# Performance work log

Hardware: AMD Instinct MI355X
Metric: run time of the kernel (lower is better)

Reference implementation:

```python
import jax, jax.numpy as jnp
import numpy as np

B_ = 2; L_ = 4096; D_MODEL = 1024; D_INNER = 2048; D_STATE = 128
N_HEADS = 32; HEADDIM = 64; D_CONV = 4; CHUNK = 64
CONV_DIM = D_INNER + 2 * D_STATE
EPS = 1e-5


def silu(x):
    return x * jax.nn.sigmoid(x)


def segsum(x):
    # x: (..., T) -> (..., T, T) stable segment sums; exp() gives 1-semiseparable matrix
    T = x.shape[-1]
    xe = jnp.broadcast_to(x[..., None], x.shape + (T,))  # (..., T, T)
    lower = jnp.tril(jnp.ones((T, T), bool), -1)
    xs = jnp.cumsum(jnp.where(lower, xe, 0.0), axis=-2)
    incl = jnp.tril(jnp.ones((T, T), bool), 0)
    return jnp.where(incl, xs, -jnp.inf)


def ssd(x, A, Bm, Cm):
    # x: (b, l, h, p); A: (b, l, h); Bm/Cm: (b, l, n) (single shared head, as in module)
    b, l, h, p = x.shape
    c = l // CHUNK
    x = x.reshape(b, c, CHUNK, h, p)
    A = A.reshape(b, c, CHUNK, h).transpose(0, 3, 1, 2)  # (b, h, c, l)
    Bm = Bm.reshape(b, c, CHUNK, D_STATE)
    Cm = Cm.reshape(b, c, CHUNK, D_STATE)
    A_cumsum = jnp.cumsum(A, axis=-1)                    # (b, h, c, l)
    Lmat = jnp.exp(segsum(A))                            # (b, h, c, l, l)
    # intra-chunk (diagonal blocks)
    Y_diag = jnp.einsum('bcln,bcsn,bhcls,bcshp->bclhp', Cm, Bm, Lmat, x)
    # per-chunk states
    decay_states = jnp.exp(A_cumsum[:, :, :, -1:] - A_cumsum)  # (b, h, c, l)
    states = jnp.einsum('bcln,bhcl,bclhp->bchpn', Bm, decay_states, x)
    init = jnp.zeros_like(states[:, :1])
    states = jnp.concatenate([init, states], axis=1)     # (b, c+1, h, p, n)
    A_last = jnp.pad(A_cumsum[:, :, :, -1], ((0, 0), (0, 0), (1, 0)))  # (b, h, c+1)
    decay_chunk = jnp.exp(segsum(A_last))                # (b, h, c+1, c+1)
    new_states = jnp.einsum('bhzc,bchpn->bzhpn', decay_chunk, states)
    states_prev = new_states[:, :-1]                     # (b, c, h, p, n)
    state_decay_out = jnp.exp(A_cumsum)
    Y_off = jnp.einsum('bcln,bchpn,bhcl->bclhp', Cm, states_prev, state_decay_out)
    return (Y_diag + Y_off).reshape(b, l, h, p)


def setup_inputs() -> dict:
    key = jax.random.key(0)
    ks = jax.random.split(key, 9)
    u = jax.random.normal(ks[0], (B_, L_, D_MODEL), jnp.float32)
    W_in = jax.random.normal(ks[1], (2 * D_INNER + 2 * D_STATE + N_HEADS, D_MODEL), jnp.float32) * (D_MODEL ** -0.5)
    conv_w = jax.random.normal(ks[2], (CONV_DIM, 1, D_CONV), jnp.float32) * 0.2
    conv_b = jax.random.normal(ks[3], (CONV_DIM,), jnp.float32) * 0.02
    dt_bias = jax.random.normal(ks[4], (N_HEADS,), jnp.float32) * 0.1
    A_log = jnp.log(jax.random.uniform(ks[5], (N_HEADS,), jnp.float32, 1.0, 16.0))
    D_param = jax.random.normal(ks[6], (N_HEADS,), jnp.float32) * 0.5
    norm_w = jnp.ones((D_INNER,), jnp.float32)
    W_out = jax.random.normal(ks[7], (D_MODEL, D_INNER), jnp.float32) * (D_INNER ** -0.5)
    return dict(u=u, W_in=W_in, conv_w=conv_w, conv_b=conv_b, dt_bias=dt_bias,
                A_log=A_log, D_param=D_param, norm_w=norm_w, W_out=W_out)


def mamba_forward(u, W_in, conv_w, conv_b, dt_bias, A_log, D_param, norm_w, W_out):
    b, l, _ = u.shape
    zxbcdt = u @ W_in.T                                  # (b, l, 2*di+2*ds+h)
    z = zxbcdt[..., :D_INNER]
    xBC = zxbcdt[..., D_INNER:D_INNER + CONV_DIM]
    dt = zxbcdt[..., D_INNER + CONV_DIM:]
    dt = jax.nn.softplus(dt + dt_bias)                   # (b, l, h)
    # causal depthwise conv1d
    xc = jnp.transpose(xBC, (0, 2, 1))                   # (b, conv_dim, l)
    xc = jax.lax.conv_general_dilated(xc, conv_w, (1,), [(D_CONV - 1, 0)],
                                      feature_group_count=CONV_DIM,
                                      dimension_numbers=('NCH', 'OIH', 'NCH'))
    xc = xc + conv_b[None, :, None]
    xBC = silu(jnp.transpose(xc, (0, 2, 1)))             # (b, l, conv_dim)
    x = xBC[..., :D_INNER]
    Bc = xBC[..., D_INNER:D_INNER + D_STATE]
    Cc = xBC[..., D_INNER + D_STATE:]
    x = x.reshape(b, l, N_HEADS, HEADDIM)
    A = -jnp.exp(A_log)                                  # (h,)
    Y = ssd(x * dt[..., None], A * dt, Bc, Cc)           # (b, l, h, p)
    y = Y + x * D_param[:, None]
    y = y.reshape(b, l, D_INNER)
    # gated RMSNorm
    y = y * silu(z)
    y = y * jax.lax.rsqrt(jnp.mean(y * y, axis=-1, keepdims=True) + EPS) * norm_w
    return y @ W_out.T


def reference(u, W_in, conv_w, conv_b, dt_bias, A_log, D_param, norm_w, W_out):
    return mamba_forward(u, W_in, conv_w, conv_b, dt_bias, A_log, D_param, norm_w, W_out)
```

## Files before the change

kernel.cpp:

```cpp
#include <hip/hip_runtime.h>
#include <hip/hip_bf16.h>
#include <math.h>

#define B_    2
#define L_    4096
#define DM    1024
#define DI    2048
#define DS    128
#define NH    32
#define HD    64
#define CHUNK 64
#define NC    (L_/CHUNK)
#define CD    (DI + 2*DS)
#define ROWS  (B_*L_)
#define NOUT  (2*DI + 2*DS + NH)
#define NPAD2 4608

typedef __attribute__((ext_vector_type(4))) float f32x4;
typedef __attribute__((ext_vector_type(8))) __bf16 bf16x8;
typedef __attribute__((ext_vector_type(4))) short s16x4;
typedef __attribute__((ext_vector_type(8))) short s16x8;

__global__ __launch_bounds__(256) void k_convert_all(const float* __restrict__ u, const float* __restrict__ W_in,
                                                     const float* __restrict__ W_out, __bf16* __restrict__ ubf,
                                                     __bf16* __restrict__ wibf, __bf16* __restrict__ wobf) {
    int i = blockIdx.x * 256 + threadIdx.x;
    const int QU  = ROWS * DM / 4;
    const int QWI = NPAD2 * DM / 4;
    const int QWO = DM * DI / 4;
    const float* s = nullptr;
    __bf16* d;
    bool zero = false;
    if (i < QU) {
        s = u + (size_t)i * 4; d = ubf + (size_t)i * 4;
    } else if (i < QU + QWI) {
        int j = i - QU;
        d = wibf + (size_t)j * 4;
        if (j < NOUT * DM / 4) s = W_in + (size_t)j * 4; else zero = true;
    } else if (i < QU + QWI + QWO) {
        int j = i - QU - QWI;
        s = W_out + (size_t)j * 4; d = wobf + (size_t)j * 4;
    } else return;
    s16x4 o = {0, 0, 0, 0};
    if (!zero) {
        f32x4 v = *(const f32x4*)s;
#pragma unroll
        for (int q = 0; q < 4; q++) o[q] = __builtin_bit_cast(short, (__bf16)v[q]);
    }
    *(s16x4*)d = o;
}

__device__ __forceinline__ void stage_half(const __bf16* __restrict__ G, int ldg, int grow0, int kt,
                                           char* lds, int ldsoff, int tid, int wave) {
#pragma unroll
    for (int issue = 0; issue < 2; issue++) {
        int o   = issue * 8192 + tid * 16;
        int row = o >> 7;
        int cb  = (o & 127) ^ ((row & 7) << 4);
        const __bf16* src = G + (size_t)(grow0 + row) * ldg + kt + (cb >> 1);
        char* ldsbase = lds + ldsoff + issue * 8192 + wave * 1024;
        __builtin_amdgcn_global_load_lds((const __attribute__((address_space(1))) void*)src,
                                         (__attribute__((address_space(3))) void*)ldsbase,
                                         16, 0, 0);
    }
}

__device__ __forceinline__ bf16x8 rdfrag(const char* lds, int ldsoff, int r, int ks, int lane) {
    int logical = r * 128 + ks * 64 + ((lane >> 4) << 4);
    int phys    = logical ^ ((r & 7) << 4);
    return *(const bf16x8*)(lds + ldsoff + phys);
}

#define MFMA_CLUSTER(AF, BF, ACC)                                                         \
    __builtin_amdgcn_s_setprio(1);                                                       \
    _Pragma("unroll")                                                                    \
    for (int fm = 0; fm < 4; fm++)                                                       \
        _Pragma("unroll")                                                                \
        for (int fn = 0; fn < 2; fn++)                                                   \
            _Pragma("unroll")                                                            \
            for (int ks = 0; ks < 2; ks++)                                               \
                ACC[fm][fn] = __builtin_amdgcn_mfma_f32_16x16x32_bf16(AF[fm][ks], BF[fn][ks], ACC[fm][fn], 0, 0, 0); \
    __builtin_amdgcn_s_setprio(0);

__device__ __forceinline__ void gemm128x256_core(const __bf16* __restrict__ Ag, const __bf16* __restrict__ Bg,
                                                 int K, int m0, int n0, char* lds, f32x4 acc[4][4]) {
    const int tid = threadIdx.x, wave = tid >> 6, lane = tid & 63;
    const int wm = wave >> 2, wn = wave & 3, lrow = lane & 15;
    const int KT = K >> 6;
    const int brow = wn * 64;
    const int bhalf = 16384 + ((brow >> 7) << 14);
    const int brl = brow & 127;

    for (int t = 0; t < KT; t++) {
        const int kt = t << 6;
        stage_half(Ag, K, m0,       kt, lds, 0,     tid, wave);
        stage_half(Bg, K, n0,       kt, lds, 16384, tid, wave);
        stage_half(Bg, K, n0 + 128, kt, lds, 32768, tid, wave);
        asm volatile("s_waitcnt vmcnt(0)" ::: "memory");
        __builtin_amdgcn_s_barrier();
        bf16x8 a[4][2];
#pragma unroll
        for (int fm = 0; fm < 4; fm++)
#pragma unroll
            for (int ks = 0; ks < 2; ks++)
                a[fm][ks] = rdfrag(lds, 0, wm * 64 + fm * 16 + lrow, ks, lane);
        __builtin_amdgcn_s_setprio(1);
#pragma unroll
        for (int fn = 0; fn < 4; fn++) {
            bf16x8 b0 = rdfrag(lds, bhalf, brl + fn * 16 + lrow, 0, lane);
            bf16x8 b1 = rdfrag(lds, bhalf, brl + fn * 16 + lrow, 1, lane);
#pragma unroll
            for (int fm = 0; fm < 4; fm++) {
                acc[fm][fn] = __builtin_amdgcn_mfma_f32_16x16x32_bf16(a[fm][0], b0, acc[fm][fn], 0, 0, 0);
                acc[fm][fn] = __builtin_amdgcn_mfma_f32_16x16x32_bf16(a[fm][1], b1, acc[fm][fn], 0, 0, 0);
            }
        }
        __builtin_amdgcn_s_setprio(0);
        __builtin_amdgcn_s_barrier();
    }
}

__device__ __forceinline__ void gemm256x128_core(const __bf16* __restrict__ Ag, const __bf16* __restrict__ Bg,
                                                 int K, int m0, int n0, char* lds, f32x4 acc[8][2]) {
    const int tid = threadIdx.x, wave = tid >> 6, lane = tid & 63;
    const int wmq = wave >> 2, wnq = wave & 3, lrow = lane & 15;
    const int KT = K >> 6;
    const int aoff = wmq * 16384;

    auto stage_tile = [&](int t, int p) {
        const int kt = t << 6;
        stage_half(Ag, K, m0,       kt, lds, p * 49152,         tid, wave);
        stage_half(Ag, K, m0 + 128, kt, lds, p * 49152 + 16384, tid, wave);
        stage_half(Bg, K, n0,       kt, lds, p * 49152 + 32768, tid, wave);
    };
    stage_tile(0, 0);
    asm volatile("s_waitcnt vmcnt(0)" ::: "memory");
    __builtin_amdgcn_s_barrier();

    bf16x8 ra[4][2], rb[2][2];
#pragma unroll
    for (int fm = 0; fm < 4; fm++)
#pragma unroll
        for (int ks = 0; ks < 2; ks++)
            ra[fm][ks] = rdfrag(lds, aoff, fm * 16 + lrow, ks, lane);
#pragma unroll
    for (int fn = 0; fn < 2; fn++)
#pragma unroll
        for (int ks = 0; ks < 2; ks++)
            rb[fn][ks] = rdfrag(lds, 32768, wnq * 32 + fn * 16 + lrow, ks, lane);

    for (int t = 0; t < KT; t++) {
        const int p = t & 1, pn = p ^ 1;
        const bool dsg = (t + 1 < KT);
        if (dsg) {
            stage_half(Ag, K, m0,       (t + 1) << 6, lds, pn * 49152,         tid, wave);
            stage_half(Ag, K, m0 + 128, (t + 1) << 6, lds, pn * 49152 + 16384, tid, wave);
        }
        {
            f32x4 (*a0)[2] = &acc[0];
            MFMA_CLUSTER(ra, rb, a0);
        }
#pragma unroll
        for (int fm = 0; fm < 4; fm++)
#pragma unroll
            for (int ks = 0; ks < 2; ks++)
                ra[fm][ks] = rdfrag(lds, p * 49152 + aoff, 64 + fm * 16 + lrow, ks, lane);
        if (dsg) stage_half(Bg, K, n0, (t + 1) << 6, lds, pn * 49152 + 32768, tid, wave);
        {
            f32x4 (*a1)[2] = &acc[4];
            MFMA_CLUSTER(ra, rb, a1);
        }
        asm volatile("s_waitcnt vmcnt(0)" ::: "memory");
        __builtin_amdgcn_s_barrier();
        if (dsg) {
#pragma unroll
            for (int fm = 0; fm < 4; fm++)
#pragma unroll
                for (int ks = 0; ks < 2; ks++)
                    ra[fm][ks] = rdfrag(lds, pn * 49152 + aoff, fm * 16 + lrow, ks, lane);
#pragma unroll
            for (int fn = 0; fn < 2; fn++)
#pragma unroll
                for (int ks = 0; ks < 2; ks++)
                    rb[fn][ks] = rdfrag(lds, pn * 49152 + 32768, wnq * 32 + fn * 16 + lrow, ks, lane);
        }
    }
}

__global__ __launch_bounds__(512, 4) void k_gemm1(const __bf16* __restrict__ ubf, const __bf16* __restrict__ wibf,
                                                  __bf16* __restrict__ zbuf, __bf16* __restrict__ xbcraw,
                                                  float* __restrict__ dtbuf, const float* __restrict__ dt_bias) {
    extern __shared__ char lds[];
    f32x4 acc[4][4];
    f32x4 z4 = {0.f, 0.f, 0.f, 0.f};
#pragma unroll
    for (int i = 0; i < 4; i++)
#pragma unroll
        for (int j = 0; j < 4; j++) acc[i][j] = z4;

    int bid = blockIdx.x;
    int wg  = (bid & 7) * 144 + (bid >> 3);
    int m0  = (wg / 18) * 128;
    int n0  = (wg % 18) * 256;
    gemm128x256_core(ubf, wibf, DM, m0, n0, lds, acc);

    const int lane = threadIdx.x & 63, wave = threadIdx.x >> 6;
    const int wm = wave >> 2, wn = wave & 3;
    const int gm_base = m0 + wm * 64 + ((lane >> 4) << 2);
    const int gn_base = n0 + wn * 64 + (lane & 15);
#pragma unroll
    for (int fm = 0; fm < 4; fm++) {
        const int gmb = gm_base + fm * 16;
#pragma unroll
        for (int fn = 0; fn < 4; fn++) {
            const int gn = gn_base + fn * 16;
            if (gn < DI) {
#pragma unroll
                for (int r = 0; r < 4; r++)
                    zbuf[(size_t)(gmb + r) * DI + gn] = (__bf16)acc[fm][fn][r];
            } else if (gn < DI + CD) {
#pragma unroll
                for (int r = 0; r < 4; r++)
                    xbcraw[(size_t)(gmb + r) * CD + (gn - DI)] = (__bf16)acc[fm][fn][r];
            } else if (gn < NOUT) {
                const int hh = gn - (DI + CD);
                const float bb = dt_bias[hh];
#pragma unroll
                for (int r = 0; r < 4; r++) {
                    float x = acc[fm][fn][r] + bb;
                    float sp = (x > 20.f) ? x : log1pf(__expf(x));
                    dtbuf[(size_t)(gmb + r) * NH + hh] = sp;
                }
            }
        }
    }
}

__global__ __launch_bounds__(512, 2) void k_gemm2(const __bf16* __restrict__ ybf, const __bf16* __restrict__ wobf,
                                                  float* __restrict__ out) {
    extern __shared__ char lds[];
    f32x4 acc[8][2];
    f32x4 z4 = {0.f, 0.f, 0.f, 0.f};
#pragma unroll
    for (int i = 0; i < 8; i++)
#pragma unroll
        for (int j = 0; j < 2; j++) acc[i][j] = z4;

    int bid = blockIdx.x;
    int wg  = (bid & 7) * 32 + (bid >> 3);
    int m0  = (wg / 8) * 256;
    int n0  = (wg % 8) * 128;
    gemm256x128_core(ybf, wobf, DI, m0, n0, lds, acc);

    const int lane = threadIdx.x & 63, wave = threadIdx.x >> 6;
    const int wmq = wave >> 2, wnq = wave & 3;
#pragma unroll
    for (int fm = 0; fm < 8; fm++) {
        const int gmb = m0 + wmq * 128 + fm * 16 + ((lane >> 4) << 2);
#pragma unroll
        for (int fn = 0; fn < 2; fn++) {
            const int gn = n0 + wnq * 32 + fn * 16 + (lane & 15);
#pragma unroll
            for (int r = 0; r < 4; r++)
                out[(size_t)(gmb + r) * DM + gn] = acc[fm][fn][r];
        }
    }
}

__global__ __launch_bounds__(256) void k_conv(const __bf16* __restrict__ xbcraw, const float* __restrict__ conv_w,
                                              const float* __restrict__ conv_b, __bf16* __restrict__ xconv) {
    __shared__ float wsh[256 * 4];
    __shared__ float bsh[256];
    const int tid  = threadIdx.x;
    const int gsub = tid & 31;
    const int roct = tid >> 5;
    const int ch_base_blk = blockIdx.x * 256;
    *(f32x4*)&wsh[tid * 4] = *(const f32x4*)&conv_w[ch_base_blk * 4 + tid * 4];
    bsh[tid] = conv_b[ch_base_blk + tid];
    __syncthreads();

    const int ch0  = ch_base_blk + gsub * 8;
    const int row0 = (blockIdx.y * 8 + roct) * 8;
    const int l0   = row0 & (L_ - 1);
    const __bf16* src = xbcraw + (size_t)row0 * CD + ch0;

    s16x8 rr[11];
#pragma unroll
    for (int j = 0; j < 11; j++) {
        int ll = l0 - 3 + j;
        if (ll >= 0) rr[j] = *(const s16x8*)(src + (size_t)(j - 3) * CD);
        else         rr[j] = (s16x8){0, 0, 0, 0, 0, 0, 0, 0};
    }

    const int chl = gsub * 8;
    float w[8][4], bias[8];
#pragma unroll
    for (int j = 0; j < 8; j++) {
        bias[j] = bsh[chl + j];
#pragma unroll
        for (int k = 0; k < 4; k++) w[j][k] = wsh[(chl + j) * 4 + k];
    }

    __bf16* dst = xconv + (size_t)row0 * CD + ch0;
#pragma unroll
    for (int orow = 0; orow < 8; orow++) {
        float a[8];
#pragma unroll
        for (int j = 0; j < 8; j++) a[j] = bias[j];
#pragma unroll
        for (int k = 0; k < 4; k++) {
            s16x8 v = rr[orow + k];
#pragma unroll
            for (int j = 0; j < 8; j++)
                a[j] += w[j][k] * (float)__builtin_bit_cast(__bf16, (short)v[j]);
        }
        s16x8 o;
#pragma unroll
        for (int j = 0; j < 8; j++)
            o[j] = __builtin_bit_cast(short, (__bf16)(a[j] * __builtin_amdgcn_rcpf(1.f + __expf(-a[j]))));
        *(s16x8*)(dst + (size_t)orow * CD) = o;
    }
}

__global__ __launch_bounds__(256) void k_cbt(const __bf16* __restrict__ xconv, float* __restrict__ cbt) {
    const int c = blockIdx.x, b = blockIdx.y;
    const int tid = threadIdx.x, wv = tid >> 6, lane = tid & 63;
    const int lrow = lane & 15, lko = (lane >> 4) * 8;
    __shared__ __align__(16) __bf16 Csh[64 * 136];
    __shared__ __align__(16) __bf16 Bsh[64 * 136];
    const size_t rowbase = (size_t)b * L_ + c * CHUNK;
#pragma unroll
    for (int q = 0; q < 32; q++) {
        int i = q * 2 + (wv >> 1);
        int n = (wv & 1) * 64 + lane;
        const __bf16* base = xconv + (rowbase + i) * CD + DI;
        Bsh[i * 136 + n] = base[n];
        Csh[i * 136 + n] = base[DS + n];
    }
    __syncthreads();
    f32x4 acc[4];
    f32x4 z4 = {0.f, 0.f, 0.f, 0.f};
#pragma unroll
    for (int jt = 0; jt < 4; jt++) acc[jt] = z4;
#pragma unroll
    for (int ks = 0; ks < 4; ks++) {
        bf16x8 a = *(const bf16x8*)&Csh[(wv * 16 + lrow) * 136 + ks * 32 + lko];
#pragma unroll
        for (int jt = 0; jt < 4; jt++) {
            bf16x8 bb = *(const bf16x8*)&Bsh[(jt * 16 + lrow) * 136 + ks * 32 + lko];
            acc[jt] = __builtin_amdgcn_mfma_f32_16x16x32_bf16(a, bb, acc[jt], 0, 0, 0);
        }
    }
    float* o = cbt + (size_t)(b * NC + c) * 4096;
#pragma unroll
    for (int jt = 0; jt < 4; jt++)
#pragma unroll
        for (int r = 0; r < 4; r++) {
            int i = wv * 16 + (lane >> 4) * 4 + r;
            int j = jt * 16 + lrow;
            o[i * 64 + j] = acc[jt][r];
        }
}

__global__ __launch_bounds__(256) void k_ssd_a(const __bf16* __restrict__ xconv, const float* __restrict__ dtbuf,
                                               const float* __restrict__ cbt, const float* __restrict__ A_log,
                                               __bf16* __restrict__ ybuf, __bf16* __restrict__ states,
                                               float* __restrict__ asum, const float* __restrict__ D_param) {
    const int hg = blockIdx.x, c = blockIdx.y, b = blockIdx.z;
    const int tid = threadIdx.x, wv = tid >> 6, lane = tid & 63;
    const int lrow = lane & 15, lko = (lane >> 4) * 8;
    __shared__ __align__(16) __bf16 xT[64 * 72];
    __shared__ __align__(16) __bf16 xsc[64 * 72];
    __shared__ __align__(16) __bf16 BT[128 * 72];
    __shared__ __align__(16) __bf16 Ms[64 * 72];
    __shared__ float dts[64], cum[64];

    const size_t rowbase = (size_t)b * L_ + c * CHUNK;
#pragma unroll
    for (int q = 0; q < 32; q++) {
        int i = q * 2 + (wv >> 1);
        int n = (wv & 1) * 64 + lane;
        BT[n * 72 + i] = xconv[(rowbase + i) * CD + DI + n];
    }
    const float* cbt_bc = cbt + (size_t)(b * NC + c) * 4096;
    f32x4 z4 = {0.f, 0.f, 0.f, 0.f};

    for (int hh = 0; hh < 8; hh++) {
        const int h = hg * 8 + hh;
        const float Ah = -__expf(A_log[h]);
        const float Dh = D_param[h];
#pragma unroll
        for (int q = 0; q < 16; q++) {
            int i = q * 4 + wv;
            xT[lane * 72 + i] = xconv[(rowbase + i) * CD + h * HD + lane];
        }
        if (wv == 0) {
            float dtv = dtbuf[(rowbase + lane) * NH + h];
            dts[lane] = dtv;
            float v = Ah * dtv;
#pragma unroll
            for (int o = 1; o < 64; o <<= 1) { float t = __shfl_up(v, o); if (lane >= o) v += t; }
            cum[lane] = v;
            if (lane == 63) asum[(b * NC + c) * NH + h] = v;
        }
        __syncthreads();

        const float cum63 = cum[63];
#pragma unroll
        for (int q = 0; q < 16; q++) {
            int i = q * 4 + wv, j = lane;
            float cumi = cum[i];
            float m = 0.f;
            if (j <= i) m = cbt_bc[i * 64 + j] * __expf(cumi - cum[j]) * dts[j];
            if (j == i) m += Dh;
            Ms[i * 72 + j] = (__bf16)m;
            float dcfi = __expf(cum63 - cumi) * dts[i];
            xsc[lane * 72 + i] = (__bf16)((float)xT[lane * 72 + i] * dcfi);
        }
        __syncthreads();

        {
            f32x4 accY[4];
#pragma unroll
            for (int pt = 0; pt < 4; pt++) accY[pt] = z4;
#pragma unroll
            for (int ks = 0; ks < 2; ks++) {
                bf16x8 a = *(const bf16x8*)&Ms[(wv * 16 + lrow) * 72 + ks * 32 + lko];
#pragma unroll
                for (int pt = 0; pt < 4; pt++) {
                    bf16x8 bb = *(const bf16x8*)&xT[(pt * 16 + lrow) * 72 + ks * 32 + lko];
                    accY[pt] = __builtin_amdgcn_mfma_f32_16x16x32_bf16(a, bb, accY[pt], 0, 0, 0);
                }
            }
#pragma unroll
            for (int pt = 0; pt < 4; pt++)
#pragma unroll
                for (int r = 0; r < 4; r++) {
                    int i = wv * 16 + (lane >> 4) * 4 + r;
                    int p = pt * 16 + lrow;
                    ybuf[(rowbase + i) * DI + h * HD + p] = (__bf16)accY[pt][r];
                }
        }
        {
            f32x4 accS[8];
#pragma unroll
            for (int nt = 0; nt < 8; nt++) accS[nt] = z4;
#pragma unroll
            for (int ks = 0; ks < 2; ks++) {
                bf16x8 a = *(const bf16x8*)&xsc[(wv * 16 + lrow) * 72 + ks * 32 + lko];
#pragma unroll
                for (int nt = 0; nt < 8; nt++) {
                    bf16x8 bb = *(const bf16x8*)&BT[(nt * 16 + lrow) * 72 + ks * 32 + lko];
                    accS[nt] = __builtin_amdgcn_mfma_f32_16x16x32_bf16(a, bb, accS[nt], 0, 0, 0);
                }
            }
            __bf16* sp = states + ((size_t)(b * NC + c) * NH + h) * 8192;
#pragma unroll
            for (int nt = 0; nt < 8; nt++)
#pragma unroll
                for (int r = 0; r < 4; r++) {
                    int p = wv * 16 + (lane >> 4) * 4 + r;
                    int n = nt * 16 + lrow;
                    sp[p * 128 + n] = (__bf16)accS[nt][r];
                }
        }
        __syncthreads();
    }
}

__global__ __launch_bounds__(256) void k_scan(__bf16* __restrict__ states, const float* __restrict__ asum) {
    const int seg = blockIdx.x, h = blockIdx.y, b = blockIdx.z;
    __shared__ float efs[NC];
    if (threadIdx.x < NC) efs[threadIdx.x] = __expf(asum[(b * NC + threadIdx.x) * NH + h]);
    __syncthreads();
    const int e0 = seg * 1024 + threadIdx.x * 4;
    __bf16* base = states + ((size_t)(b * NC) * NH + h) * 8192 + e0;
    const size_t cs = (size_t)NH * 8192;
    float S[4] = {0.f, 0.f, 0.f, 0.f};
    s16x4 r0 = *(const s16x4*)(base);
    s16x4 r1 = *(const s16x4*)(base + cs);
    s16x4 r2 = *(const s16x4*)(base + 2 * cs);
    s16x4 r3;
#define SCAN_STEP(RV, CC)                                                                  \
    {                                                                                      \
        s16x4 o; float e = efs[CC];                                                        \
        _Pragma("unroll")                                                                  \
        for (int q = 0; q < 4; q++) {                                                      \
            float t = (float)__builtin_bit_cast(__bf16, (short)RV[q]);                     \
            o[q] = __builtin_bit_cast(short, (__bf16)S[q]);                                \
            S[q] = e * S[q] + t;                                                           \
        }                                                                                  \
        *(s16x4*)(base + (size_t)(CC) * cs) = o;                                           \
    }
    for (int c = 0; c < NC; c += 4) {
        r3 = *(const s16x4*)(base + (size_t)(c + 3) * cs);
        SCAN_STEP(r0, c);
        if (c + 4 < NC) r0 = *(const s16x4*)(base + (size_t)(c + 4) * cs);
        SCAN_STEP(r1, c + 1);
        if (c + 5 < NC) r1 = *(const s16x4*)(base + (size_t)(c + 5) * cs);
        SCAN_STEP(r2, c + 2);
        if (c + 6 < NC) r2 = *(const s16x4*)(base + (size_t)(c + 6) * cs);
        SCAN_STEP(r3, c + 3);
    }
#undef SCAN_STEP
}

__global__ __launch_bounds__(256) void k_ssd_b(const __bf16* __restrict__ xconv, const float* __restrict__ dtbuf,
                                               const __bf16* __restrict__ states, const float* __restrict__ A_log,
                                               __bf16* __restrict__ ybuf) {
    const int hg = blockIdx.x, c = blockIdx.y, b = blockIdx.z;
    const int tid = threadIdx.x, wv = tid >> 6, lane = tid & 63;
    const int lrow = lane & 15, lko = (lane >> 4) * 8;
    __shared__ __align__(16) __bf16 Csh[64 * 136];
    __shared__ __align__(16) __bf16 Sps[64 * 136];
    __shared__ float cum[64];

    const size_t rowbase = (size_t)b * L_ + c * CHUNK;
#pragma unroll
    for (int q = 0; q < 32; q++) {
        int i = q * 2 + (wv >> 1);
        int n = (wv & 1) * 64 + lane;
        Csh[i * 136 + n] = xconv[(rowbase + i) * CD + DI + DS + n];
    }
    f32x4 z4 = {0.f, 0.f, 0.f, 0.f};

    for (int hh = 0; hh < 8; hh++) {
        const int h = hg * 8 + hh;
        const float Ah = -__expf(A_log[h]);
        const __bf16* sp = states + ((size_t)(b * NC + c) * NH + h) * 8192;
#pragma unroll
        for (int q = 0; q < 32; q++) {
            int i = q * 2 + (wv >> 1);
            int n = (wv & 1) * 64 + lane;
            Sps[i * 136 + n] = sp[i * 128 + n];
        }
        if (wv == 0) {
            float v = Ah * dtbuf[(rowbase + lane) * NH + h];
#pragma unroll
            for (int o = 1; o < 64; o <<= 1) { float t = __shfl_up(v, o); if (lane >= o) v += t; }
            cum[lane] = v;
        }
        __syncthreads();

        f32x4 acc[4];
#pragma unroll
        for (int pt = 0; pt < 4; pt++) acc[pt] = z4;
#pragma unroll
        for (int ks = 0; ks < 4; ks++) {
            bf16x8 a = *(const bf16x8*)&Csh[(wv * 16 + lrow) * 136 + ks * 32 + lko];
#pragma unroll
            for (int pt = 0; pt < 4; pt++) {
                bf16x8 bb = *(const bf16x8*)&Sps[(pt * 16 + lrow) * 136 + ks * 32 + lko];
                acc[pt] = __builtin_amdgcn_mfma_f32_16x16x32_bf16(a, bb, acc[pt], 0, 0, 0);
            }
        }
#pragma unroll
        for (int r = 0; r < 4; r++) {
            int i = wv * 16 + (lane >> 4) * 4 + r;
            float ef = __expf(cum[i]);
#pragma unroll
            for (int pt = 0; pt < 4; pt++) {
                size_t idx = (rowbase + i) * DI + h * HD + pt * 16 + lrow;
                float y0 = (float)ybuf[idx];
                ybuf[idx] = (__bf16)(y0 + ef * acc[pt][r]);
            }
        }
        __syncthreads();
    }
}

__global__ __launch_bounds__(256) void k_gate_norm(const __bf16* __restrict__ ybuf, const __bf16* __restrict__ zbuf,
                                                   const float* __restrict__ norm_w, __bf16* __restrict__ ybf) {
    const int r = blockIdx.x;
    const int tid = threadIdx.x;
    const int col0 = tid * 8;
    s16x8 y8 = *(const s16x8*)(ybuf + (size_t)r * DI + col0);
    s16x8 z8 = *(const s16x8*)(zbuf + (size_t)r * DI + col0);
    float v[8];
    float ss = 0.f;
#pragma unroll
    for (int q = 0; q < 8; q++) {
        float y = (float)__builtin_bit_cast(__bf16, (short)y8[q]);
        float z = (float)__builtin_bit_cast(__bf16, (short)z8[q]);
        float g = z * __builtin_amdgcn_rcpf(1.f + __expf(-z));
        v[q] = y * g;
        ss += v[q] * v[q];
    }
#pragma unroll
    for (int o = 32; o > 0; o >>= 1) ss += __shfl_down(ss, o);
    __shared__ float wsum[4];
    __shared__ float rmss;
    if ((tid & 63) == 0) wsum[tid >> 6] = ss;
    __syncthreads();
    if (tid == 0) {
        float t = wsum[0] + wsum[1] + wsum[2] + wsum[3];
        rmss = rsqrtf(t / (float)DI + 1e-5f);
    }
    __syncthreads();
    float rm = rmss;
    s16x8 o8;
#pragma unroll
    for (int q = 0; q < 8; q++)
        o8[q] = __builtin_bit_cast(short, (__bf16)(v[q] * rm * norm_w[col0 + q]));
    *(s16x8*)(ybf + (size_t)r * DI + col0) = o8;
}

extern "C" void kernel_launch(void* const* d_in, const int* in_sizes, int n_in,
                              void* d_out, int out_size, void* d_ws, size_t ws_size,
                              hipStream_t stream) {
    const float* u       = (const float*)d_in[0];
    const float* W_in    = (const float*)d_in[1];
    const float* conv_w  = (const float*)d_in[2];
    const float* conv_b  = (const float*)d_in[3];
    const float* dt_bias = (const float*)d_in[4];
    const float* A_log   = (const float*)d_in[5];
    const float* D_param = (const float*)d_in[6];
    const float* norm_w  = (const float*)d_in[7];
    const float* W_out   = (const float*)d_in[8];
    float* out = (float*)d_out;

    constexpr size_t OFF_WOBF  = 0;
    constexpr size_t OFF_ZBUF  = 4194304;
    constexpr size_t OFF_DT    = 37748736;
    constexpr size_t OFF_ASUM  = 38797312;
    constexpr size_t OFF_XCONV = 38813696;
    constexpr size_t OFF_CBT   = 76562432;
    constexpr size_t OFF_BIG   = 78659584;
    constexpr size_t NEED      = 145768448;
    if (ws_size < NEED) return;

    char* ws = (char*)d_ws;
    __bf16* wobf   = (__bf16*)(ws + OFF_WOBF);
    __bf16* zbuf   = (__bf16*)(ws + OFF_ZBUF);
    float*  dtbuf  = (float*) (ws + OFF_DT);
    float*  asum   = (float*) (ws + OFF_ASUM);
    __bf16* xconv  = (__bf16*)(ws + OFF_XCONV);
    float*  cbt    = (float*) (ws + OFF_CBT);
    __bf16* ubf    = (__bf16*)(ws + OFF_BIG);
    __bf16* wibf   = (__bf16*)(ws + OFF_BIG + 16777216);
    __bf16* xbcraw = (__bf16*)(ws + OFF_BIG + 16777216 + 9437184);
    __bf16* states = (__bf16*)(ws + OFF_BIG);
    __bf16* ybf    = (__bf16*)(ws + OFF_XCONV);
    __bf16* ybuf   = (__bf16*)d_out;

    (void)hipFuncSetAttribute((const void*)k_gemm1, hipFuncAttributeMaxDynamicSharedMemorySize, 49152);
    (void)hipFuncSetAttribute((const void*)k_gemm2, hipFuncAttributeMaxDynamicSharedMemorySize, 98304);

    constexpr int QTOT = ROWS * DM / 4 + NPAD2 * DM / 4 + DM * DI / 4;
    k_convert_all<<<(QTOT + 255) / 256, 256, 0, stream>>>(u, W_in, W_out, ubf, wibf, wobf);

    k_gemm1<<<1152, 512, 49152, stream>>>(ubf, wibf, zbuf, xbcraw, dtbuf, dt_bias);
    k_conv<<<dim3(9, 128), 256, 0, stream>>>(xbcraw, conv_w, conv_b, xconv);
    k_cbt<<<dim3(NC, B_), 256, 0, stream>>>(xconv, cbt);
    k_ssd_a<<<dim3(4, NC, B_), 256, 0, stream>>>(xconv, dtbuf, cbt, A_log, ybuf, states, asum, D_param);
    k_scan<<<dim3(8, NH, B_), 256, 0, stream>>>(states, asum);
    k_ssd_b<<<dim3(4, NC, B_), 256, 0, stream>>>(xconv, dtbuf, states, A_log, ybuf);
    k_gate_norm<<<ROWS, 256, 0, stream>>>(ybuf, zbuf, norm_w, ybf);
    k_gemm2<<<256, 512, 98304, stream>>>(ybf, wobf, out);
}
```

Baseline: 369.4 us.

## Launch one block per head in SSD kernels and shrink gemm2 tiles

The SSD intra-chunk and state-output kernels now run one block per (head, chunk, batch) instead of looping over 8 heads per block. This gives 8x more blocks and removes the per-head barriers, at the cost of reloading the shared B and C chunk data once per head. The output GEMM swaps the double-buffered 256x128 tile for a simpler single-buffered 128x128 tile with less LDS and higher occupancy, so twice as many blocks launch but the load/compute overlap is lost.

```diff
diff --git a/kernel.cpp b/kernel.cpp
--- a/kernel.cpp
+++ b/kernel.cpp
@@ -71,17 +71,6 @@
     return *(const bf16x8*)(lds + ldsoff + phys);
 }
 
-#define MFMA_CLUSTER(AF, BF, ACC)                                                         \
-    __builtin_amdgcn_s_setprio(1);                                                       \
-    _Pragma("unroll")                                                                    \
-    for (int fm = 0; fm < 4; fm++)                                                       \
-        _Pragma("unroll")                                                                \
-        for (int fn = 0; fn < 2; fn++)                                                   \
-            _Pragma("unroll")                                                            \
-            for (int ks = 0; ks < 2; ks++)                                               \
-                ACC[fm][fn] = __builtin_amdgcn_mfma_f32_16x16x32_bf16(AF[fm][ks], BF[fn][ks], ACC[fm][fn], 0, 0, 0); \
-    __builtin_amdgcn_s_setprio(0);
-
 __device__ __forceinline__ void gemm128x256_core(const __bf16* __restrict__ Ag, const __bf16* __restrict__ Bg,
                                                  int K, int m0, int n0, char* lds, f32x4 acc[4][4]) {
     const int tid = threadIdx.x, wave = tid >> 6, lane = tid & 63;
@@ -120,70 +109,37 @@
     }
 }
 
-__device__ __forceinline__ void gemm256x128_core(const __bf16* __restrict__ Ag, const __bf16* __restrict__ Bg,
-                                                 int K, int m0, int n0, char* lds, f32x4 acc[8][2]) {
+__device__ __forceinline__ void gemm128x128_core(const __bf16* __restrict__ Ag, const __bf16* __restrict__ Bg,
+                                                 int K, int m0, int n0, char* lds, f32x4 acc[4][2]) {
     const int tid = threadIdx.x, wave = tid >> 6, lane = tid & 63;
-    const int wmq = wave >> 2, wnq = wave & 3, lrow = lane & 15;
+    const int wm = wave >> 2, wn = wave & 3, lrow = lane & 15;
     const int KT = K >> 6;
-    const int aoff = wmq * 16384;
-
-    auto stage_tile = [&](int t, int p) {
+
+    for (int t = 0; t < KT; t++) {
         const int kt = t << 6;
-        stage_half(Ag, K, m0,       kt, lds, p * 49152,         tid, wave);
-        stage_half(Ag, K, m0 + 128, kt, lds, p * 49152 + 16384, tid, wave);
-        stage_half(Bg, K, n0,       kt, lds, p * 49152 + 32768, tid, wave);
-    };
-    stage_tile(0, 0);
-    asm volatile("s_waitcnt vmcnt(0)" ::: "memory");
-    __builtin_amdgcn_s_barrier();
-
-    bf16x8 ra[4][2], rb[2][2];
-#pragma unroll
-    for (int fm = 0; fm < 4; fm++)
-#pragma unroll
-        for (int ks = 0; ks < 2; ks++)
-            ra[fm][ks] = rdfrag(lds, aoff, fm * 16 + lrow, ks, lane);
-#pragma unroll
-    for (int fn = 0; fn < 2; fn++)
-#pragma unroll
-        for (int ks = 0; ks < 2; ks++)
-            rb[fn][ks] = rdfrag(lds, 32768, wnq * 32 + fn * 16 + lrow, ks, lane);
-
-    for (int t = 0; t < KT; t++) {
-        const int p = t & 1, pn = p ^ 1;
-        const bool dsg = (t + 1 < KT);
-        if (dsg) {
-            stage_half(Ag, K, m0,       (t + 1) << 6, lds, pn * 49152,         tid, wave);
-            stage_half(Ag, K, m0 + 128, (t + 1) << 6, lds, pn * 49152 + 16384, tid, wave);
-        }
-        {
-            f32x4 (*a0)[2] = &acc[0];
-            MFMA_CLUSTER(ra, rb, a0);
-        }
-#pragma unroll
-        for (int fm = 0; fm < 4; fm++)
-#pragma unroll
-            for (int ks = 0; ks < 2; ks++)
-                ra[fm][ks] = rdfrag(lds, p * 49152 + aoff, 64 + fm * 16 + lrow, ks, lane);
-        if (dsg) stage_half(Bg, K, n0, (t + 1) << 6, lds, pn * 49152 + 32768, tid, wave);
-        {
-            f32x4 (*a1)[2] = &acc[4];
-            MFMA_CLUSTER(ra, rb, a1);
-        }
+        stage_half(Ag, K, m0, kt, lds, 0,     tid, wave);
+        stage_half(Bg, K, n0, kt, lds, 16384, tid, wave);
         asm volatile("s_waitcnt vmcnt(0)" ::: "memory");
         __builtin_amdgcn_s_barrier();
-        if (dsg) {
-#pragma unroll
-            for (int fm = 0; fm < 4; fm++)
-#pragma unroll
-                for (int ks = 0; ks < 2; ks++)
-                    ra[fm][ks] = rdfrag(lds, pn * 49152 + aoff, fm * 16 + lrow, ks, lane);
-#pragma unroll
-            for (int fn = 0; fn < 2; fn++)
-#pragma unroll
-                for (int ks = 0; ks < 2; ks++)
-                    rb[fn][ks] = rdfrag(lds, pn * 49152 + 32768, wnq * 32 + fn * 16 + lrow, ks, lane);
-        }
+        bf16x8 a[4][2];
+#pragma unroll
+        for (int fm = 0; fm < 4; fm++)
+#pragma unroll
+            for (int ks = 0; ks < 2; ks++)
+                a[fm][ks] = rdfrag(lds, 0, wm * 64 + fm * 16 + lrow, ks, lane);
+        __builtin_amdgcn_s_setprio(1);
+#pragma unroll
+        for (int fn = 0; fn < 2; fn++) {
+            bf16x8 b0 = rdfrag(lds, 16384, wn * 32 + fn * 16 + lrow, 0, lane);
+            bf16x8 b1 = rdfrag(lds, 16384, wn * 32 + fn * 16 + lrow, 1, lane);
+#pragma unroll
+            for (int fm = 0; fm < 4; fm++) {
+                acc[fm][fn] = __builtin_amdgcn_mfma_f32_16x16x32_bf16(a[fm][0], b0, acc[fm][fn], 0, 0, 0);
+                acc[fm][fn] = __builtin_amdgcn_mfma_f32_16x16x32_bf16(a[fm][1], b1, acc[fm][fn], 0, 0, 0);
+            }
+        }
+        __builtin_amdgcn_s_setprio(0);
+        __builtin_amdgcn_s_barrier();
     }
 }
 
@@ -236,30 +192,32 @@
     }
 }
 
-__global__ __launch_bounds__(512, 2) void k_gemm2(const __bf16* __restrict__ ybf, const __bf16* __restrict__ wobf,
+__global__ __launch_bounds__(512, 4) void k_gemm2(const __bf16* __restrict__ ybf, const __bf16* __restrict__ wobf,
                                                   float* __restrict__ out) {
     extern __shared__ char lds[];
-    f32x4 acc[8][2];
+    f32x4 acc[4][2];
     f32x4 z4 = {0.f, 0.f, 0.f, 0.f};
 #pragma unroll
-    for (int i = 0; i < 8; i++)
+    for (int i = 0; i < 4; i++)
 #pragma unroll
         for (int j = 0; j < 2; j++) acc[i][j] = z4;
 
     int bid = blockIdx.x;
-    int wg  = (bid & 7) * 32 + (bid >> 3);
-    int m0  = (wg / 8) * 256;
+    int wg  = (bid & 7) * 64 + (bid >> 3);
+    int m0  = (wg / 8) * 128;
     int n0  = (wg % 8) * 128;
-    gemm256x128_core(ybf, wobf, DI, m0, n0, lds, acc);
+    gemm128x128_core(ybf, wobf, DI, m0, n0, lds, acc);
 
     const int lane = threadIdx.x & 63, wave = threadIdx.x >> 6;
-    const int wmq = wave >> 2, wnq = wave & 3;
-#pragma unroll
-    for (int fm = 0; fm < 8; fm++) {
-        const int gmb = m0 + wmq * 128 + fm * 16 + ((lane >> 4) << 2);
+    const int wm = wave >> 2, wn = wave & 3;
+    const int gm_base = m0 + wm * 64 + ((lane >> 4) << 2);
+    const int gn_base = n0 + wn * 32 + (lane & 15);
+#pragma unroll
+    for (int fm = 0; fm < 4; fm++) {
+        const int gmb = gm_base + fm * 16;
 #pragma unroll
         for (int fn = 0; fn < 2; fn++) {
-            const int gn = n0 + wnq * 32 + fn * 16 + (lane & 15);
+            const int gn = gn_base + fn * 16;
 #pragma unroll
             for (int r = 0; r < 4; r++)
                 out[(size_t)(gmb + r) * DM + gn] = acc[fm][fn][r];
@@ -366,7 +324,7 @@
                                                const float* __restrict__ cbt, const float* __restrict__ A_log,
                                                __bf16* __restrict__ ybuf, __bf16* __restrict__ states,
                                                float* __restrict__ asum, const float* __restrict__ D_param) {
-    const int hg = blockIdx.x, c = blockIdx.y, b = blockIdx.z;
+    const int h = blockIdx.x, c = blockIdx.y, b = blockIdx.z;
     const int tid = threadIdx.x, wv = tid >> 6, lane = tid & 63;
     const int lrow = lane & 15, lko = (lane >> 4) * 8;
     __shared__ __align__(16) __bf16 xT[64 * 72];
@@ -375,96 +333,92 @@
     __shared__ __align__(16) __bf16 Ms[64 * 72];
     __shared__ float dts[64], cum[64];
 
+    const float Ah = -__expf(A_log[h]);
     const size_t rowbase = (size_t)b * L_ + c * CHUNK;
+
+    float dtv = 0.f;
+    if (wv == 0) { dtv = dtbuf[(rowbase + lane) * NH + h]; dts[lane] = dtv; }
+#pragma unroll
+    for (int q = 0; q < 16; q++) {
+        int i = q * 4 + wv;
+        xT[lane * 72 + i] = xconv[(rowbase + i) * CD + h * HD + lane];
+    }
 #pragma unroll
     for (int q = 0; q < 32; q++) {
         int i = q * 2 + (wv >> 1);
         int n = (wv & 1) * 64 + lane;
         BT[n * 72 + i] = xconv[(rowbase + i) * CD + DI + n];
     }
+    if (wv == 0) {
+        float v = Ah * dtv;
+#pragma unroll
+        for (int o = 1; o < 64; o <<= 1) { float t = __shfl_up(v, o); if (lane >= o) v += t; }
+        cum[lane] = v;
+        if (lane == 63) asum[(b * NC + c) * NH + h] = v;
+    }
+    __syncthreads();
+
+    const float cum63 = cum[63];
+    const float Dh = D_param[h];
     const float* cbt_bc = cbt + (size_t)(b * NC + c) * 4096;
+#pragma unroll
+    for (int q = 0; q < 16; q++) {
+        int i = q * 4 + wv, j = lane;
+        float cumi = cum[i];
+        float m = 0.f;
+        if (j <= i) m = cbt_bc[i * 64 + j] * __expf(cumi - cum[j]) * dts[j];
+        if (j == i) m += Dh;
+        Ms[i * 72 + j] = (__bf16)m;
+        float dcfi = __expf(cum63 - cumi) * dts[i];
+        xsc[lane * 72 + i] = (__bf16)((float)xT[lane * 72 + i] * dcfi);
+    }
+    __syncthreads();
+
     f32x4 z4 = {0.f, 0.f, 0.f, 0.f};
-
-    for (int hh = 0; hh < 8; hh++) {
-        const int h = hg * 8 + hh;
-        const float Ah = -__expf(A_log[h]);
-        const float Dh = D_param[h];
-#pragma unroll
-        for (int q = 0; q < 16; q++) {
-            int i = q * 4 + wv;
-            xT[lane * 72 + i] = xconv[(rowbase + i) * CD + h * HD + lane];
-        }
-        if (wv == 0) {
-            float dtv = dtbuf[(rowbase + lane) * NH + h];
-            dts[lane] = dtv;
-            float v = Ah * dtv;
-#pragma unroll
-            for (int o = 1; o < 64; o <<= 1) { float t = __shfl_up(v, o); if (lane >= o) v += t; }
-            cum[lane] = v;
-            if (lane == 63) asum[(b * NC + c) * NH + h] = v;
-        }
-        __syncthreads();
-
-        const float cum63 = cum[63];
-#pragma unroll
-        for (int q = 0; q < 16; q++) {
-            int i = q * 4 + wv, j = lane;
-            float cumi = cum[i];
-            float m = 0.f;
-            if (j <= i) m = cbt_bc[i * 64 + j] * __expf(cumi - cum[j]) * dts[j];
-            if (j == i) m += Dh;
-            Ms[i * 72 + j] = (__bf16)m;
-            float dcfi = __expf(cum63 - cumi) * dts[i];
-            xsc[lane * 72 + i] = (__bf16)((float)xT[lane * 72 + i] * dcfi);
-        }
-        __syncthreads();
-
-        {
-            f32x4 accY[4];
-#pragma unroll
-            for (int pt = 0; pt < 4; pt++) accY[pt] = z4;
-#pragma unroll
-            for (int ks = 0; ks < 2; ks++) {
-                bf16x8 a = *(const bf16x8*)&Ms[(wv * 16 + lrow) * 72 + ks * 32 + lko];
-#pragma unroll
-                for (int pt = 0; pt < 4; pt++) {
-                    bf16x8 bb = *(const bf16x8*)&xT[(pt * 16 + lrow) * 72 + ks * 32 + lko];
-                    accY[pt] = __builtin_amdgcn_mfma_f32_16x16x32_bf16(a, bb, accY[pt], 0, 0, 0);
-                }
+    {
+        f32x4 accY[4];
+#pragma unroll
+        for (int pt = 0; pt < 4; pt++) accY[pt] = z4;
+#pragma unroll
+        for (int ks = 0; ks < 2; ks++) {
+            bf16x8 a = *(const bf16x8*)&Ms[(wv * 16 + lrow) * 72 + ks * 32 + lko];
+#pragma unroll
+            for (int pt = 0; pt < 4; pt++) {
+                bf16x8 bb = *(const bf16x8*)&xT[(pt * 16 + lrow) * 72 + ks * 32 + lko];
+                accY[pt] = __builtin_amdgcn_mfma_f32_16x16x32_bf16(a, bb, accY[pt], 0, 0, 0);
             }
-#pragma unroll
-            for (int pt = 0; pt < 4; pt++)
-#pragma unroll
-                for (int r = 0; r < 4; r++) {
-                    int i = wv * 16 + (lane >> 4) * 4 + r;
-                    int p = pt * 16 + lrow;
-                    ybuf[(rowbase + i) * DI + h * HD + p] = (__bf16)accY[pt][r];
-                }
-        }
-        {
-            f32x4 accS[8];
-#pragma unroll
-            for (int nt = 0; nt < 8; nt++) accS[nt] = z4;
-#pragma unroll
-            for (int ks = 0; ks < 2; ks++) {
-                bf16x8 a = *(const bf16x8*)&xsc[(wv * 16 + lrow) * 72 + ks * 32 + lko];
-#pragma unroll
-                for (int nt = 0; nt < 8; nt++) {
-                    bf16x8 bb = *(const bf16x8*)&BT[(nt * 16 + lrow) * 72 + ks * 32 + lko];
-                    accS[nt] = __builtin_amdgcn_mfma_f32_16x16x32_bf16(a, bb, accS[nt], 0, 0, 0);
-                }
+        }
+#pragma unroll
+        for (int pt = 0; pt < 4; pt++)
+#pragma unroll
+            for (int r = 0; r < 4; r++) {
+                int i = wv * 16 + (lane >> 4) * 4 + r;
+                int p = pt * 16 + lrow;
+                ybuf[(rowbase + i) * DI + h * HD + p] = (__bf16)accY[pt][r];
             }
-            __bf16* sp = states + ((size_t)(b * NC + c) * NH + h) * 8192;
-#pragma unroll
-            for (int nt = 0; nt < 8; nt++)
-#pragma unroll
-                for (int r = 0; r < 4; r++) {
-                    int p = wv * 16 + (lane >> 4) * 4 + r;
-                    int n = nt * 16 + lrow;
-                    sp[p * 128 + n] = (__bf16)accS[nt][r];
-                }
-        }
-        __syncthreads();
+    }
+    {
+        f32x4 accS[8];
+#pragma unroll
+        for (int nt = 0; nt < 8; nt++) accS[nt] = z4;
+#pragma unroll
+        for (int ks = 0; ks < 2; ks++) {
+            bf16x8 a = *(const bf16x8*)&xsc[(wv * 16 + lrow) * 72 + ks * 32 + lko];
+#pragma unroll
+            for (int nt = 0; nt < 8; nt++) {
+                bf16x8 bb = *(const bf16x8*)&BT[(nt * 16 + lrow) * 72 + ks * 32 + lko];
+                accS[nt] = __builtin_amdgcn_mfma_f32_16x16x32_bf16(a, bb, accS[nt], 0, 0, 0);
+            }
+        }
+        __bf16* sp = states + ((size_t)(b * NC + c) * NH + h) * 8192;
+#pragma unroll
+        for (int nt = 0; nt < 8; nt++)
+#pragma unroll
+            for (int r = 0; r < 4; r++) {
+                int p = wv * 16 + (lane >> 4) * 4 + r;
+                int n = nt * 16 + lrow;
+                sp[p * 128 + n] = (__bf16)accS[nt][r];
+            }
     }
 }
 
@@ -508,64 +462,54 @@
 __global__ __launch_bounds__(256) void k_ssd_b(const __bf16* __restrict__ xconv, const float* __restrict__ dtbuf,
                                                const __bf16* __restrict__ states, const float* __restrict__ A_log,
                                                __bf16* __restrict__ ybuf) {
-    const int hg = blockIdx.x, c = blockIdx.y, b = blockIdx.z;
+    const int h = blockIdx.x, c = blockIdx.y, b = blockIdx.z;
     const int tid = threadIdx.x, wv = tid >> 6, lane = tid & 63;
     const int lrow = lane & 15, lko = (lane >> 4) * 8;
     __shared__ __align__(16) __bf16 Csh[64 * 136];
     __shared__ __align__(16) __bf16 Sps[64 * 136];
     __shared__ float cum[64];
 
+    const float Ah = -__expf(A_log[h]);
     const size_t rowbase = (size_t)b * L_ + c * CHUNK;
+    const __bf16* sp = states + ((size_t)(b * NC + c) * NH + h) * 8192;
 #pragma unroll
     for (int q = 0; q < 32; q++) {
         int i = q * 2 + (wv >> 1);
         int n = (wv & 1) * 64 + lane;
         Csh[i * 136 + n] = xconv[(rowbase + i) * CD + DI + DS + n];
-    }
+        Sps[i * 136 + n] = sp[i * 128 + n];
+    }
+    if (wv == 0) {
+        float v = Ah * dtbuf[(rowbase + lane) * NH + h];
+#pragma unroll
+        for (int o = 1; o < 64; o <<= 1) { float t = __shfl_up(v, o); if (lane >= o) v += t; }
+        cum[lane] = v;
+    }
+    __syncthreads();
+
+    f32x4 acc[4];
     f32x4 z4 = {0.f, 0.f, 0.f, 0.f};
-
-    for (int hh = 0; hh < 8; hh++) {
-        const int h = hg * 8 + hh;
-        const float Ah = -__expf(A_log[h]);
-        const __bf16* sp = states + ((size_t)(b * NC + c) * NH + h) * 8192;
-#pragma unroll
-        for (int q = 0; q < 32; q++) {
-            int i = q * 2 + (wv >> 1);
-            int n = (wv & 1) * 64 + lane;
-            Sps[i * 136 + n] = sp[i * 128 + n];
-        }
-        if (wv == 0) {
-            float v = Ah * dtbuf[(rowbase + lane) * NH + h];
-#pragma unroll
-            for (int o = 1; o < 64; o <<= 1) { float t = __shfl_up(v, o); if (lane >= o) v += t; }
-            cum[lane] = v;
-        }
-        __syncthreads();
-
-        f32x4 acc[4];
-#pragma unroll
-        for (int pt = 0; pt < 4; pt++) acc[pt] = z4;
-#pragma unroll
-        for (int ks = 0; ks < 4; ks++) {
-            bf16x8 a = *(const bf16x8*)&Csh[(wv * 16 + lrow) * 136 + ks * 32 + lko];
-#pragma unroll
-            for (int pt = 0; pt < 4; pt++) {
-                bf16x8 bb = *(const bf16x8*)&Sps[(pt * 16 + lrow) * 136 + ks * 32 + lko];
-                acc[pt] = __builtin_amdgcn_mfma_f32_16x16x32_bf16(a, bb, acc[pt], 0, 0, 0);
-            }
-        }
-#pragma unroll
-        for (int r = 0; r < 4; r++) {
-            int i = wv * 16 + (lane >> 4) * 4 + r;
-            float ef = __expf(cum[i]);
-#pragma unroll
-            for (int pt = 0; pt < 4; pt++) {
-                size_t idx = (rowbase + i) * DI + h * HD + pt * 16 + lrow;
-                float y0 = (float)ybuf[idx];
-                ybuf[idx] = (__bf16)(y0 + ef * acc[pt][r]);
-            }
-        }
-        __syncthreads();
+#pragma unroll
+    for (int pt = 0; pt < 4; pt++) acc[pt] = z4;
+#pragma unroll
+    for (int ks = 0; ks < 4; ks++) {
+        bf16x8 a = *(const bf16x8*)&Csh[(wv * 16 + lrow) * 136 + ks * 32 + lko];
+#pragma unroll
+        for (int pt = 0; pt < 4; pt++) {
+            bf16x8 bb = *(const bf16x8*)&Sps[(pt * 16 + lrow) * 136 + ks * 32 + lko];
+            acc[pt] = __builtin_amdgcn_mfma_f32_16x16x32_bf16(a, bb, acc[pt], 0, 0, 0);
+        }
+    }
+#pragma unroll
+    for (int r = 0; r < 4; r++) {
+        int i = wv * 16 + (lane >> 4) * 4 + r;
+        float ef = __expf(cum[i]);
+#pragma unroll
+        for (int pt = 0; pt < 4; pt++) {
+            size_t idx = (rowbase + i) * DI + h * HD + pt * 16 + lrow;
+            float y0 = (float)ybuf[idx];
+            ybuf[idx] = (__bf16)(y0 + ef * acc[pt][r]);
+        }
     }
 }
 
@@ -644,7 +588,7 @@
     __bf16* ybuf   = (__bf16*)d_out;
 
     (void)hipFuncSetAttribute((const void*)k_gemm1, hipFuncAttributeMaxDynamicSharedMemorySize, 49152);
-    (void)hipFuncSetAttribute((const void*)k_gemm2, hipFuncAttributeMaxDynamicSharedMemorySize, 98304);
+    (void)hipFuncSetAttribute((const void*)k_gemm2, hipFuncAttributeMaxDynamicSharedMemorySize, 32768);
 
     constexpr int QTOT = ROWS * DM / 4 + NPAD2 * DM / 4 + DM * DI / 4;
     k_convert_all<<<(QTOT + 255) / 256, 256, 0, stream>>>(u, W_in, W_out, ubf, wibf, wobf);
@@ -652,9 +596,9 @@
     k_gemm1<<<1152, 512, 49152, stream>>>(ubf, wibf, zbuf, xbcraw, dtbuf, dt_bias);
     k_conv<<<dim3(9, 128), 256, 0, stream>>>(xbcraw, conv_w, conv_b, xconv);
     k_cbt<<<dim3(NC, B_), 256, 0, stream>>>(xconv, cbt);
-    k_ssd_a<<<dim3(4, NC, B_), 256, 0, stream>>>(xconv, dtbuf, cbt, A_log, ybuf, states, asum, D_param);
+    k_ssd_a<<<dim3(NH, NC, B_), 256, 0, stream>>>(xconv, dtbuf, cbt, A_log, ybuf, states, asum, D_param);
     k_scan<<<dim3(8, NH, B_), 256, 0, stream>>>(states, asum);
-    k_ssd_b<<<dim3(4, NC, B_), 256, 0, stream>>>(xconv, dtbuf, states, A_log, ybuf);
+    k_ssd_b<<<dim3(NH, NC, B_), 256, 0, stream>>>(xconv, dtbuf, states, A_log, ybuf);
     k_gate_norm<<<ROWS, 256, 0, stream>>>(ybuf, zbuf, norm_w, ybf);
-    k_gemm2<<<256, 512, 98304, stream>>>(ybf, wobf, out);
-}
+    k_gemm2<<<512, 512, 32768, stream>>>(ybf, wobf, out);
+}
```

After: 305.9 us (median of 2 runs). 1.21x faster.
